# Kernel optimization log

Measured on AMD Instinct MI355X. Metric: run time of the kernel, lower is better.

The kernel has to match this reference:

```python
import jax, jax.numpy as jnp
import numpy as np

HEADS = 4
OUT_DIM = 64
NEG_SLOPE = 0.2


def setup_inputs() -> dict:
    key = jax.random.key(0)
    k1, k2, k3, k4 = jax.random.split(key, 4)
    n, in_dim = 4096, 256
    x = jax.random.normal(k1, (n, in_dim), dtype=jnp.float32)
    adj = jax.random.randint(k2, (n, n), 0, 2, dtype=jnp.int32)
    # lin: in_dim -> heads*out_dim (no bias), stored as [in_dim, heads*out_dim]
    W = jax.random.normal(k3, (in_dim, HEADS * OUT_DIM), dtype=jnp.float32) * 0.05
    # att_weight: [heads, 2*out_dim]
    att = jax.random.normal(k4, (HEADS, 2 * OUT_DIM), dtype=jnp.float32) * 0.05
    return {"x": x, "adj": adj, "W": W, "att": att}


def reference(x, adj, W, att):
    n = x.shape[0]
    h = (x @ W).reshape(n, HEADS, OUT_DIM)  # [n, H, D]
    # scores[i,j,h] = att[h] . cat(h_i, h_j) = <h_i, a_src[h]> + <h_j, a_dst[h]>
    a_src, a_dst = att[:, :OUT_DIM], att[:, OUT_DIM:]
    e_src = jnp.einsum('nhd,hd->nh', h, a_src)  # [n, H]
    e_dst = jnp.einsum('nhd,hd->nh', h, a_dst)  # [n, H]
    scores = e_src[:, None, :] + e_dst[None, :, :]  # [n, n, H]
    scores = jax.nn.leaky_relu(scores, negative_slope=NEG_SLOPE)
    mask = (adj > 0)[:, :, None]  # [n, n, 1]
    scores = jnp.where(mask, scores, -jnp.inf)
    alpha = jax.nn.softmax(scores, axis=1)  # softmax over neighbors j
    # h_prime[i,h,d] = sum_j alpha[i,j,h] * h[j,h,d]
    h_prime = jnp.einsum('ijh,jhd->ihd', alpha, h)
    return h_prime.reshape(n, HEADS * OUT_DIM)
```

## Files before the change

kernel.cpp:

```cpp
#include <hip/hip_runtime.h>
#include <hip/hip_bf16.h>

#define HEADS 4
#define ODIM 64
#define HD 256
#define NEG_SLOPE 0.2f
#define SPLITS 4
#define BJ 128

typedef __attribute__((ext_vector_type(8))) short bf16x8;
typedef __attribute__((ext_vector_type(4))) float floatx4;
typedef __attribute__((ext_vector_type(2))) float floatx2;

__global__ __launch_bounds__(256) void pack_xw(const float* __restrict__ x,
                                               const float* __restrict__ W,
                                               __hip_bfloat16* __restrict__ xh,
                                               __hip_bfloat16* __restrict__ xl,
                                               __hip_bfloat16* __restrict__ wh,
                                               __hip_bfloat16* __restrict__ wl,
                                               int K, int nxb) {
    const int b = blockIdx.x;
    const int Kc = K >> 5;
    if (b < nxb) {
        const int g = b * 256 + threadIdx.x;
        const int lane = g & 63, frag = g >> 6;
        const int kc = frag % Kc, mc = frag / Kc;
        const int l16 = lane & 15, q = lane >> 4;
        const float* src = x + (size_t)(mc * 16 + l16) * K + kc * 32 + q * 8;
        const float4 v0 = *(const float4*)src;
        const float4 v1 = *(const float4*)(src + 4);
        const float vv[8] = {v0.x, v0.y, v0.z, v0.w, v1.x, v1.y, v1.z, v1.w};
        union { __hip_bfloat16 b[8]; bf16x8 v; } H, L;
        #pragma unroll
        for (int p = 0; p < 8; ++p) {
            H.b[p] = __float2bfloat16(vv[p]);
            L.b[p] = __float2bfloat16(vv[p] - __bfloat162float(H.b[p]));
        }
        *(bf16x8*)&xh[(size_t)frag * 512 + lane * 8] = H.v;
        *(bf16x8*)&xl[(size_t)frag * 512 + lane * 8] = L.v;
    } else {
        const int g = (b - nxb) * 256 + threadIdx.x;
        const int lane = g & 63, frag = g >> 6;
        const int kc = frag % Kc, nc = frag / Kc;
        const int l16 = lane & 15, q = lane >> 4;
        union { __hip_bfloat16 b[8]; bf16x8 v; } H, L;
        #pragma unroll
        for (int p = 0; p < 8; ++p) {
            const float w = W[(size_t)(kc * 32 + q * 8 + p) * HD + nc * 16 + l16];
            H.b[p] = __float2bfloat16(w);
            L.b[p] = __float2bfloat16(w - __bfloat162float(H.b[p]));
        }
        *(bf16x8*)&wh[(size_t)frag * 512 + lane * 8] = H.v;
        *(bf16x8*)&wl[(size_t)frag * 512 + lane * 8] = L.v;
    }
}

__global__ __launch_bounds__(128) void gemm_fused(
    const __hip_bfloat16* __restrict__ xh, const __hip_bfloat16* __restrict__ xl,
    const __hip_bfloat16* __restrict__ wh, const __hip_bfloat16* __restrict__ wl,
    const float* __restrict__ att, float4* __restrict__ E4,
    __hip_bfloat16* __restrict__ hbB, int n, int K) {

    __shared__ __hip_bfloat16 T[64][40];

    const int tid = threadIdx.x, wave = tid >> 6, lane = tid & 63;
    const int q = lane >> 4, l16 = lane & 15;
    const int m0 = blockIdx.x * 32;
    const int head = blockIdx.y;
    const int Kc = K >> 5;
    const int mc = (m0 >> 4) + wave;

    floatx4 acc[4] = {{0.f,0.f,0.f,0.f},{0.f,0.f,0.f,0.f},{0.f,0.f,0.f,0.f},{0.f,0.f,0.f,0.f}};

    const __hip_bfloat16* Axh = xh + (size_t)mc * Kc * 512 + lane * 8;
    const __hip_bfloat16* Axl = xl + (size_t)mc * Kc * 512 + lane * 8;
    const __hip_bfloat16* Bwh = wh + lane * 8;
    const __hip_bfloat16* Bwl = wl + lane * 8;
    #pragma unroll 2
    for (int kc = 0; kc < Kc; ++kc) {
        const bf16x8 ah = *(const bf16x8*)(Axh + (size_t)kc * 512);
        const bf16x8 al = *(const bf16x8*)(Axl + (size_t)kc * 512);
        bf16x8 bh[4], bl[4];
        #pragma unroll
        for (int nt = 0; nt < 4; ++nt) {
            const size_t fo = (size_t)((head * 4 + nt) * Kc + kc) * 512;
            bh[nt] = *(const bf16x8*)(Bwh + fo);
            bl[nt] = *(const bf16x8*)(Bwl + fo);
        }
        #pragma unroll
        for (int nt = 0; nt < 4; ++nt)
            acc[nt] = __builtin_amdgcn_mfma_f32_16x16x32_bf16(ah, bh[nt], acc[nt], 0, 0, 0);
        #pragma unroll
        for (int nt = 0; nt < 4; ++nt)
            acc[nt] = __builtin_amdgcn_mfma_f32_16x16x32_bf16(ah, bl[nt], acc[nt], 0, 0, 0);
        #pragma unroll
        for (int nt = 0; nt < 4; ++nt)
            acc[nt] = __builtin_amdgcn_mfma_f32_16x16x32_bf16(al, bh[nt], acc[nt], 0, 0, 0);
    }

    float as_v[4], ad_v[4];
    #pragma unroll
    for (int nt = 0; nt < 4; ++nt) {
        as_v[nt] = att[head * 2 * ODIM + nt * 16 + l16];
        ad_v[nt] = att[head * 2 * ODIM + ODIM + nt * 16 + l16];
    }
    #pragma unroll
    for (int r = 0; r < 4; ++r) {
        float ps = 0.f, pd = 0.f;
        #pragma unroll
        for (int nt = 0; nt < 4; ++nt) {
            ps = fmaf(acc[nt][r], as_v[nt], ps);
            pd = fmaf(acc[nt][r], ad_v[nt], pd);
        }
        #pragma unroll
        for (int m = 1; m <= 8; m <<= 1) {
            ps += __shfl_xor(ps, m, 64);
            pd += __shfl_xor(pd, m, 64);
        }
        if (l16 == 0) {
            const int i = m0 + wave * 16 + q * 4 + r;
            E4[i * HEADS + head] = make_float4(__expf(ps), __expf(NEG_SLOPE * ps),
                                               __expf(pd), __expf(NEG_SLOPE * pd));
        }
    }

    #pragma unroll
    for (int nt = 0; nt < 4; ++nt) {
        union { __hip_bfloat16 b[4]; uint2 u; } pk;
        #pragma unroll
        for (int r = 0; r < 4; ++r) pk.b[r] = __float2bfloat16(acc[nt][r]);
        *(uint2*)&T[nt * 16 + l16][wave * 16 + q * 4] = pk.u;
    }
    __syncthreads();

    #pragma unroll
    for (int ffi = 0; ffi < 2; ++ffi) {
        const int f = wave + ffi * 2;
        const bf16x8 v = *(const bf16x8*)&T[f * 16 + l16][q * 8];
        const size_t frag = ((size_t)head * (n >> 5) + (m0 >> 5)) * 4 + f;
        *(bf16x8*)&hbB[frag * 512 + lane * 8] = v;
    }
}

__global__ __launch_bounds__(256, 2) void aggregate(
    const int* __restrict__ adj, const float4* __restrict__ E4,
    const __hip_bfloat16* __restrict__ hbB, float* __restrict__ outsp,
    float* __restrict__ densp, int n, int KR) {

    __shared__ unsigned short adjL[2][32][136];
    __shared__ float2 EdL[2][HEADS][BJ];

    const int tid = threadIdx.x;
    const int wave = tid >> 6, lane = tid & 63;
    const int q = lane >> 4, l16 = lane & 15, q8 = (lane >> 4) * 8;
    const int i0 = blockIdx.x * 32;
    const int K0 = blockIdx.y * KR;

    const int sr = tid >> 3, sg = (tid & 7) * 16;
    const int je = tid >> 1, heb = (tid & 1) * 2;

    floatx2 es12[2];
    #pragma unroll
    for (int mt = 0; mt < 2; ++mt) {
        const float4 e = E4[(i0 + mt * 16 + l16) * HEADS + wave];
        es12[mt][0] = e.x; es12[mt][1] = e.y;
    }

    union { short s[8]; bf16x8 v; } bones;
    #pragma unroll
    for (int p = 0; p < 8; ++p) bones.s[p] = (l16 == 0) ? (short)0x3F80 : (short)0;

    floatx4 acc[2][4];
    floatx4 accd[2];
    #pragma unroll
    for (int mt = 0; mt < 2; ++mt) {
        accd[mt] = (floatx4){0.f, 0.f, 0.f, 0.f};
        #pragma unroll
        for (int nt = 0; nt < 4; ++nt) acc[mt][nt] = (floatx4){0.f, 0.f, 0.f, 0.f};
    }

    const int* aprow = &adj[(size_t)(i0 + sr) * n];
    const size_t fragbase = (size_t)wave * (n >> 5) * 4;

    int4 ajA[4], ajB[4];
    float4 evA0, evA1, evB0, evB1;

    auto loadPref = [&](int jc, int4* aj, float4& e0, float4& e1) {
        const int4* ap = (const int4*)(aprow + jc + sg);
        aj[0] = ap[0]; aj[1] = ap[1]; aj[2] = ap[2]; aj[3] = ap[3];
        e0 = E4[(jc + je) * HEADS + heb];
        e1 = E4[(jc + je) * HEADS + heb + 1];
    };
    auto stage = [&](int buf, const int4* aj, const float4& e0, const float4& e1) {
        const int* av = (const int*)aj;
        #pragma unroll
        for (int g2 = 0; g2 < 2; ++g2) {
            uint4 u;
            u.x = (av[g2*8+0] > 0 ? 0xFFFFu : 0u) | (av[g2*8+1] > 0 ? 0xFFFF0000u : 0u);
            u.y = (av[g2*8+2] > 0 ? 0xFFFFu : 0u) | (av[g2*8+3] > 0 ? 0xFFFF0000u : 0u);
            u.z = (av[g2*8+4] > 0 ? 0xFFFFu : 0u) | (av[g2*8+5] > 0 ? 0xFFFF0000u : 0u);
            u.w = (av[g2*8+6] > 0 ? 0xFFFFu : 0u) | (av[g2*8+7] > 0 ? 0xFFFF0000u : 0u);
            *(uint4*)&adjL[buf][sr][sg + g2 * 8] = u;
        }
        EdL[buf][heb][je]     = make_float2(e0.z, e0.w);
        EdL[buf][heb + 1][je] = make_float2(e1.z, e1.w);
    };

    auto computeChunk = [&](int buf, int jc) {
        bf16x8 bA[4], bB[4];
        #pragma unroll
        for (int nt = 0; nt < 4; ++nt)
            bA[nt] = *(const bf16x8*)&hbB[(fragbase + (size_t)(jc >> 5) * 4 + nt) * 512 + lane * 8];
        #pragma unroll
        for (int ks = 0; ks < 4; ++ks) {
            const bf16x8* bcur = (ks & 1) ? bB : bA;
            bf16x8* bnxt = (ks & 1) ? bA : bB;
            if (ks < 3) {
                #pragma unroll
                for (int nt = 0; nt < 4; ++nt)
                    bnxt[nt] = *(const bf16x8*)&hbB[(fragbase + (size_t)((jc >> 5) + ks + 1) * 4 + nt) * 512 + lane * 8];
            }
            const float4* ep = (const float4*)&EdL[buf][wave][ks * 32 + q8];
            const float4 e01 = ep[0], e23 = ep[1], e45 = ep[2], e67 = ep[3];
            floatx2 ed[8];
            ed[0][0]=e01.x; ed[0][1]=e01.y;  ed[1][0]=e01.z; ed[1][1]=e01.w;
            ed[2][0]=e23.x; ed[2][1]=e23.y;  ed[3][0]=e23.z; ed[3][1]=e23.w;
            ed[4][0]=e45.x; ed[4][1]=e45.y;  ed[5][0]=e45.z; ed[5][1]=e45.w;
            ed[6][0]=e67.x; ed[6][1]=e67.y;  ed[7][0]=e67.z; ed[7][1]=e67.w;
            #pragma unroll
            for (int mt = 0; mt < 2; ++mt) {
                const uint4 msk = *(const uint4*)&adjL[buf][mt * 16 + l16][ks * 32 + q8];
                const unsigned int mm[4] = {msk.x, msk.y, msk.z, msk.w};
                union { unsigned int u[4]; bf16x8 v; } af;
                #pragma unroll
                for (int p = 0; p < 4; ++p) {
                    const floatx2 pa = es12[mt] * ed[2 * p];
                    const floatx2 pb = es12[mt] * ed[2 * p + 1];
                    const float wa = fmaxf(pa[0], pa[1]);
                    const float wb = fmaxf(pb[0], pb[1]);
                    af.u[p] = __builtin_amdgcn_perm(__float_as_uint(wb), __float_as_uint(wa),
                                                    0x07060302u) & mm[p];
                }
                #pragma unroll
                for (int nt = 0; nt < 4; ++nt)
                    acc[mt][nt] = __builtin_amdgcn_mfma_f32_16x16x32_bf16(af.v, bcur[nt], acc[mt][nt], 0, 0, 0);
                accd[mt] = __builtin_amdgcn_mfma_f32_16x16x32_bf16(af.v, bones.v, accd[mt], 0, 0, 0);
            }
        }
    };

    const int KEND = K0 + KR;
    loadPref(K0, ajA, evA0, evA1);
    loadPref(K0 + BJ < KEND ? K0 + BJ : K0, ajB, evB0, evB1);
    stage(0, ajA, evA0, evA1);
    __syncthreads();

    for (int jc = K0; jc < KEND; jc += 2 * BJ) {
        int j2 = jc + 2 * BJ; if (j2 >= KEND) j2 = K0;
        loadPref(j2, ajA, evA0, evA1);
        computeChunk(0, jc);
        stage(1, ajB, evB0, evB1);
        __syncthreads();

        int j3 = jc + 3 * BJ; if (j3 >= KEND) j3 = K0;
        loadPref(j3, ajB, evB0, evB1);
        computeChunk(1, jc + BJ);
        stage(0, ajA, evA0, evA1);
        __syncthreads();
    }

    const size_t sOut = (size_t)blockIdx.y * n * HD;
    #pragma unroll
    for (int mt = 0; mt < 2; ++mt)
        #pragma unroll
        for (int nt = 0; nt < 4; ++nt)
            #pragma unroll
            for (int r = 0; r < 4; ++r)
                outsp[sOut + (size_t)(i0 + mt * 16 + q * 4 + r) * HD + wave * ODIM + nt * 16 + l16] = acc[mt][nt][r];
    if (l16 == 0) {
        #pragma unroll
        for (int mt = 0; mt < 2; ++mt)
            #pragma unroll
            for (int r = 0; r < 4; ++r)
                densp[((size_t)blockIdx.y * n + i0 + mt * 16 + q * 4 + r) * HEADS + wave] = accd[mt][r];
    }
}

__global__ __launch_bounds__(256) void normalize(const float* __restrict__ outsp,
                                                 const float* __restrict__ densp,
                                                 float* __restrict__ out, int n, int splits) {
    const int g = blockIdx.x * 256 + threadIdx.x;
    const int i = g >> 6;
    const int c4 = (g & 63) * 4;
    const int head = c4 >> 6;
    float den = 0.f;
    for (int s = 0; s < splits; ++s) den += densp[((size_t)s * n + i) * HEADS + head];
    float4 v = {0.f, 0.f, 0.f, 0.f};
    for (int s = 0; s < splits; ++s) {
        const float4 t = *(const float4*)&outsp[(size_t)s * n * HD + (size_t)i * HD + c4];
        v.x += t.x; v.y += t.y; v.z += t.z; v.w += t.w;
    }
    const float inv = 1.0f / den;
    v.x *= inv; v.y *= inv; v.z *= inv; v.w *= inv;
    *(float4*)&out[(size_t)i * HD + c4] = v;
}

extern "C" void kernel_launch(void* const* d_in, const int* in_sizes, int n_in,
                              void* d_out, int out_size, void* d_ws, size_t ws_size,
                              hipStream_t stream) {
    const float* x   = (const float*)d_in[0];
    const int*   adj = (const int*)d_in[1];
    const float* W   = (const float*)d_in[2];
    const float* att = (const float*)d_in[3];
    float* out = (float*)d_out;

    const int in_dim = in_sizes[2] / HD;
    const int n = in_sizes[0] / in_dim;

    char* ws = (char*)d_ws;
    size_t off = 0;
    auto alloc = [&](size_t bytes) -> void* {
        void* p = ws + off; off += (bytes + 255) & ~(size_t)255; return p;
    };
    __hip_bfloat16* xh = (__hip_bfloat16*)alloc((size_t)n * in_dim * 2);
    __hip_bfloat16* xl = (__hip_bfloat16*)alloc((size_t)n * in_dim * 2);
    __hip_bfloat16* wh = (__hip_bfloat16*)alloc((size_t)in_dim * HD * 2);
    __hip_bfloat16* wl = (__hip_bfloat16*)alloc((size_t)in_dim * HD * 2);
    float4*         E4 = (float4*)alloc((size_t)n * HEADS * 16);
    __hip_bfloat16* hbB = (__hip_bfloat16*)alloc((size_t)n * HD * 2);

    const size_t outB = (size_t)n * HD * 4, denB = (size_t)n * HEADS * 4;
    float* densp = (float*)alloc((size_t)SPLITS * denB);
    float* outsp = (float*)alloc((size_t)SPLITS * outB);

    const int nxb = (n / 16) * (in_dim / 32) * 64 / 256;
    const int nwb = (HD / 16) * (in_dim / 32) * 64 / 256;
    pack_xw<<<nxb + nwb, 256, 0, stream>>>(x, W, xh, xl, wh, wl, in_dim, nxb);
    gemm_fused<<<dim3(n / 32, HEADS), 128, 0, stream>>>(xh, xl, wh, wl, att, E4, hbB, n, in_dim);
    aggregate<<<dim3(n / 32, SPLITS), 256, 0, stream>>>(adj, E4, hbB, outsp, densp, n, n / SPLITS);
    normalize<<<n * 64 / 256, 256, 0, stream>>>(outsp, densp, out, n, SPLITS);
}
```

Baseline: 144.0 us.

## Pre-pack adjacency into bitmasks with ballot before aggregation

Adds a phase to the pack kernel that reads each int32 adjacency row once and compresses it into 64-bit ballot bitmasks. The aggregate kernel then loads one 32-bit word per thread per chunk instead of sixteen ints and expands the bits into the shared-memory mask. The full 64MB adjacency is still read once, but the aggregate loop's global traffic and register pressure for mask prefetch shrink. The cost is an extra bitmask write and read plus more blocks in the pack launch.

```diff
diff --git a/kernel.cpp b/kernel.cpp
--- a/kernel.cpp
+++ b/kernel.cpp
@@ -14,11 +14,13 @@
 
 __global__ __launch_bounds__(256) void pack_xw(const float* __restrict__ x,
                                                const float* __restrict__ W,
+                                               const int* __restrict__ adj,
                                                __hip_bfloat16* __restrict__ xh,
                                                __hip_bfloat16* __restrict__ xl,
                                                __hip_bfloat16* __restrict__ wh,
                                                __hip_bfloat16* __restrict__ wl,
-                                               int K, int nxb) {
+                                               unsigned long long* __restrict__ adjP,
+                                               int K, int n, int nxb, int nwb) {
     const int b = blockIdx.x;
     const int Kc = K >> 5;
     if (b < nxb) {
@@ -38,7 +40,7 @@
         }
         *(bf16x8*)&xh[(size_t)frag * 512 + lane * 8] = H.v;
         *(bf16x8*)&xl[(size_t)frag * 512 + lane * 8] = L.v;
-    } else {
+    } else if (b < nxb + nwb) {
         const int g = (b - nxb) * 256 + threadIdx.x;
         const int lane = g & 63, frag = g >> 6;
         const int kc = frag % Kc, nc = frag / Kc;
@@ -52,6 +54,18 @@
         }
         *(bf16x8*)&wh[(size_t)frag * 512 + lane * 8] = H.v;
         *(bf16x8*)&wl[(size_t)frag * 512 + lane * 8] = L.v;
+    } else {
+        const int row = b - nxb - nwb;
+        const int wv = threadIdx.x >> 6, ln = threadIdx.x & 63;
+        const int* ar = adj + (size_t)row * n;
+        unsigned long long* dst = adjP + (size_t)row * (n >> 6);
+        #pragma unroll 4
+        for (int s = 0; s < 16; ++s) {
+            const int seg = wv * 16 + s;
+            const int v = ar[seg * 64 + ln];
+            const unsigned long long m = __ballot(v > 0);
+            if (ln == 0) dst[seg] = m;
+        }
     }
 }
 
@@ -143,7 +157,7 @@
 }
 
 __global__ __launch_bounds__(256, 2) void aggregate(
-    const int* __restrict__ adj, const float4* __restrict__ E4,
+    const unsigned int* __restrict__ adjP32, const float4* __restrict__ E4,
     const __hip_bfloat16* __restrict__ hbB, float* __restrict__ outsp,
     float* __restrict__ densp, int n, int KR) {
 
@@ -156,7 +170,7 @@
     const int i0 = blockIdx.x * 32;
     const int K0 = blockIdx.y * KR;
 
-    const int sr = tid >> 3, sg = (tid & 7) * 16;
+    const int r8 = tid >> 3, seg = tid & 7;
     const int je = tid >> 1, heb = (tid & 1) * 2;
 
     floatx2 es12[2];
@@ -179,28 +193,27 @@
         for (int nt = 0; nt < 4; ++nt) acc[mt][nt] = (floatx4){0.f, 0.f, 0.f, 0.f};
     }
 
-    const int* aprow = &adj[(size_t)(i0 + sr) * n];
+    const unsigned int* aP = adjP32 + (size_t)(i0 + r8) * (n >> 5);
     const size_t fragbase = (size_t)wave * (n >> 5) * 4;
 
-    int4 ajA[4], ajB[4];
+    unsigned int awA, awB;
     float4 evA0, evA1, evB0, evB1;
 
-    auto loadPref = [&](int jc, int4* aj, float4& e0, float4& e1) {
-        const int4* ap = (const int4*)(aprow + jc + sg);
-        aj[0] = ap[0]; aj[1] = ap[1]; aj[2] = ap[2]; aj[3] = ap[3];
+    auto loadPref = [&](int jc, unsigned int& aw, float4& e0, float4& e1) {
+        aw = aP[(jc >> 5) + (seg >> 1)];
         e0 = E4[(jc + je) * HEADS + heb];
         e1 = E4[(jc + je) * HEADS + heb + 1];
     };
-    auto stage = [&](int buf, const int4* aj, const float4& e0, const float4& e1) {
-        const int* av = (const int*)aj;
+    auto stage = [&](int buf, unsigned int aw, const float4& e0, const float4& e1) {
+        const unsigned int bits = aw >> ((seg & 1) * 16);
         #pragma unroll
         for (int g2 = 0; g2 < 2; ++g2) {
             uint4 u;
-            u.x = (av[g2*8+0] > 0 ? 0xFFFFu : 0u) | (av[g2*8+1] > 0 ? 0xFFFF0000u : 0u);
-            u.y = (av[g2*8+2] > 0 ? 0xFFFFu : 0u) | (av[g2*8+3] > 0 ? 0xFFFF0000u : 0u);
-            u.z = (av[g2*8+4] > 0 ? 0xFFFFu : 0u) | (av[g2*8+5] > 0 ? 0xFFFF0000u : 0u);
-            u.w = (av[g2*8+6] > 0 ? 0xFFFFu : 0u) | (av[g2*8+7] > 0 ? 0xFFFF0000u : 0u);
-            *(uint4*)&adjL[buf][sr][sg + g2 * 8] = u;
+            u.x = ((bits >> (g2*8+0)) & 1u ? 0xFFFFu : 0u) | ((bits >> (g2*8+1)) & 1u ? 0xFFFF0000u : 0u);
+            u.y = ((bits >> (g2*8+2)) & 1u ? 0xFFFFu : 0u) | ((bits >> (g2*8+3)) & 1u ? 0xFFFF0000u : 0u);
+            u.z = ((bits >> (g2*8+4)) & 1u ? 0xFFFFu : 0u) | ((bits >> (g2*8+5)) & 1u ? 0xFFFF0000u : 0u);
+            u.w = ((bits >> (g2*8+6)) & 1u ? 0xFFFFu : 0u) | ((bits >> (g2*8+7)) & 1u ? 0xFFFF0000u : 0u);
+            *(uint4*)&adjL[buf][r8][seg * 16 + g2 * 8] = u;
         }
         EdL[buf][heb][je]     = make_float2(e0.z, e0.w);
         EdL[buf][heb + 1][je] = make_float2(e1.z, e1.w);
@@ -250,22 +263,22 @@
     };
 
     const int KEND = K0 + KR;
-    loadPref(K0, ajA, evA0, evA1);
-    loadPref(K0 + BJ < KEND ? K0 + BJ : K0, ajB, evB0, evB1);
-    stage(0, ajA, evA0, evA1);
+    loadPref(K0, awA, evA0, evA1);
+    loadPref(K0 + BJ < KEND ? K0 + BJ : K0, awB, evB0, evB1);
+    stage(0, awA, evA0, evA1);
     __syncthreads();
 
     for (int jc = K0; jc < KEND; jc += 2 * BJ) {
         int j2 = jc + 2 * BJ; if (j2 >= KEND) j2 = K0;
-        loadPref(j2, ajA, evA0, evA1);
+        loadPref(j2, awA, evA0, evA1);
         computeChunk(0, jc);
-        stage(1, ajB, evB0, evB1);
+        stage(1, awB, evB0, evB1);
         __syncthreads();
 
         int j3 = jc + 3 * BJ; if (j3 >= KEND) j3 = K0;
-        loadPref(j3, ajB, evB0, evB1);
+        loadPref(j3, awB, evB0, evB1);
         computeChunk(1, jc + BJ);
-        stage(0, ajA, evA0, evA1);
+        stage(0, awA, evA0, evA1);
         __syncthreads();
     }
 
@@ -328,6 +341,7 @@
     __hip_bfloat16* wl = (__hip_bfloat16*)alloc((size_t)in_dim * HD * 2);
     float4*         E4 = (float4*)alloc((size_t)n * HEADS * 16);
     __hip_bfloat16* hbB = (__hip_bfloat16*)alloc((size_t)n * HD * 2);
+    unsigned long long* adjP = (unsigned long long*)alloc((size_t)n * (n >> 6) * 8);
 
     const size_t outB = (size_t)n * HD * 4, denB = (size_t)n * HEADS * 4;
     float* densp = (float*)alloc((size_t)SPLITS * denB);
@@ -335,8 +349,9 @@
 
     const int nxb = (n / 16) * (in_dim / 32) * 64 / 256;
     const int nwb = (HD / 16) * (in_dim / 32) * 64 / 256;
-    pack_xw<<<nxb + nwb, 256, 0, stream>>>(x, W, xh, xl, wh, wl, in_dim, nxb);
+    const int nab = n;
+    pack_xw<<<nxb + nwb + nab, 256, 0, stream>>>(x, W, adj, xh, xl, wh, wl, adjP, in_dim, n, nxb, nwb);
     gemm_fused<<<dim3(n / 32, HEADS), 128, 0, stream>>>(xh, xl, wh, wl, att, E4, hbB, n, in_dim);
-    aggregate<<<dim3(n / 32, SPLITS), 256, 0, stream>>>(adj, E4, hbB, outsp, densp, n, n / SPLITS);
+    aggregate<<<dim3(n / 32, SPLITS), 256, 0, stream>>>((const unsigned int*)adjP, E4, hbB, outsp, densp, n, n / SPLITS);
     normalize<<<n * 64 / 256, 256, 0, stream>>>(outsp, densp, out, n, SPLITS);
 }
```

New measurement: 158.5 us. 1.1x slower.
